# Optimization experiments

Measured on AMD Instinct MI355X. Metric: run time of the kernel, lower is better.

Reference implementation:

```python
import jax, jax.numpy as jnp
import numpy as np

N_EMBD = 1024
N_HEAD = 16
HEAD_SIZE = 64
BLOCK_SIZE = 2048


def setup_inputs() -> dict:
    key = jax.random.key(0)
    ks = jax.random.split(key, 5)
    B, T = 2, 2048
    s_attn = 1.0 / np.sqrt(N_EMBD)
    x = jax.random.normal(ks[0], (B, T, N_EMBD), dtype=jnp.float32)
    W_attn = jax.random.normal(ks[1], (N_EMBD, 3 * N_EMBD), dtype=jnp.float32) * s_attn
    b_attn = jnp.zeros((3 * N_EMBD,), dtype=jnp.float32)
    W_proj = jax.random.normal(ks[2], (N_EMBD, N_EMBD), dtype=jnp.float32) * s_attn
    b_proj = jnp.zeros((N_EMBD,), dtype=jnp.float32)
    return {"x": x, "W_attn": W_attn, "b_attn": b_attn, "W_proj": W_proj, "b_proj": b_proj}


def reference(x, W_attn, b_attn, W_proj, b_proj):
    B, T, C = x.shape
    H, D = N_HEAD, HEAD_SIZE
    qkv = x @ W_attn + b_attn                      # [B, T, 3C]
    q, k, v = jnp.split(qkv, 3, axis=-1)
    # [B, H, T, D]
    q = q.reshape(B, T, H, D).transpose(0, 2, 1, 3)
    k = k.reshape(B, T, H, D).transpose(0, 2, 1, 3)
    v = v.reshape(B, T, H, D).transpose(0, 2, 1, 3)
    scores = jnp.einsum("bhqd,bhkd->bhqk", q, k) / jnp.sqrt(jnp.float32(D))
    causal = jnp.tril(jnp.ones((T, T), dtype=bool))
    scores = jnp.where(causal[None, None, :, :], scores, -jnp.inf)
    weights = jax.nn.softmax(scores, axis=-1)
    attn = jnp.einsum("bhqk,bhkd->bhqd", weights, v)  # [B, H, T, D]
    attn = attn.transpose(0, 2, 1, 3).reshape(B, T, C)
    return attn @ W_proj + b_proj
```

## Files before the change

### kernel.cpp

```cpp
#include <hip/hip_runtime.h>
#include <hip/hip_bf16.h>

#define NE 1024
#define NH 16
#define HD 64
#define TSEQ 2048
#define BATCH 2

typedef __attribute__((ext_vector_type(8))) short bf16x8;
typedef __attribute__((ext_vector_type(4))) float f32x4;
typedef __attribute__((ext_vector_type(4))) unsigned int u32x4;
typedef unsigned short u16;
typedef unsigned int u32;

__device__ inline u16 f2bf(float f) {
    __hip_bfloat16 h = __float2bfloat16(f);
    return *reinterpret_cast<u16*>(&h);
}

__device__ inline u32 cvt_pk_bf16(float lo, float hi) {
    u32 r;
    asm("v_cvt_pk_bf16_f32 %0, %1, %2" : "=v"(r) : "v"(lo), "v"(hi));
    return r;
}

#define GLD16(gptr, lptr)                                                        \
    __builtin_amdgcn_global_load_lds(                                            \
        (const __attribute__((address_space(1))) void*)(gptr),                   \
        (__attribute__((address_space(3))) void*)(lptr), 16, 0, 0)

__global__ void k_f32_to_bf16(const float* __restrict__ in, u16* __restrict__ out, int n4) {
    int i = blockIdx.x * blockDim.x + threadIdx.x;
    int stride = gridDim.x * blockDim.x;
    for (; i < n4; i += stride) {
        float4 v = reinterpret_cast<const float4*>(in)[i];
        ushort4 o;
        o.x = f2bf(v.x); o.y = f2bf(v.y); o.z = f2bf(v.z); o.w = f2bf(v.w);
        reinterpret_cast<ushort4*>(out)[i] = o;
    }
}

__global__ void k_transpose_bf16(const float* __restrict__ in, u16* __restrict__ out,
                                 int K, int N) {
    __shared__ float tile[32][33];
    int bn = blockIdx.x * 32;
    int bk = blockIdx.y * 32;
    int tx = threadIdx.x, ty = threadIdx.y;
#pragma unroll
    for (int i = 0; i < 32; i += 8)
        tile[ty + i][tx] = in[(size_t)(bk + ty + i) * N + bn + tx];
    __syncthreads();
#pragma unroll
    for (int i = 0; i < 32; i += 8)
        out[(size_t)(bn + ty + i) * K + bk + tx] = f2bf(tile[tx][ty + i]);
}

template <int MODE>
__global__ __launch_bounds__(256, 2) void k_gemm_bt(
    const u16* __restrict__ A, const u16* __restrict__ Bt,
    const float* __restrict__ bias, void* __restrict__ outp,
    int M, int N, int K) {
    __shared__ __align__(16) u16 As[128 * 32];
    __shared__ __align__(16) u16 Bs[128 * 32];
    const int l = threadIdx.x & 63;
    const int w = threadIdx.x >> 6;
    const int m0 = blockIdx.x * 128;
    const int n0 = blockIdx.y * 128;
    const int wr = w >> 1, wc = w & 1;

    f32x4 acc[4][4] = {};
    const int nkt = K >> 5;
    for (int kt = 0; kt < nkt; ++kt) {
        __syncthreads();
#pragma unroll
        for (int i = 0; i < 2; ++i) {
            int c = w * 2 + i;
            const u16* gA = A + (size_t)(m0 + c * 16 + (l >> 2)) * K + (kt << 5) + (l & 3) * 8;
            const u16* gB = Bt + (size_t)(n0 + c * 16 + (l >> 2)) * K + (kt << 5) + (l & 3) * 8;
            GLD16(gA, As + c * 512);
            GLD16(gB, Bs + c * 512);
        }
        __syncthreads();
        bf16x8 af[4], bfr[4];
#pragma unroll
        for (int mi = 0; mi < 4; ++mi)
            af[mi] = *reinterpret_cast<const bf16x8*>(As + (wr * 64 + mi * 16 + (l & 15)) * 32 + (l >> 4) * 8);
#pragma unroll
        for (int ni = 0; ni < 4; ++ni)
            bfr[ni] = *reinterpret_cast<const bf16x8*>(Bs + (wc * 64 + ni * 16 + (l & 15)) * 32 + (l >> 4) * 8);
#pragma unroll
        for (int mi = 0; mi < 4; ++mi)
#pragma unroll
            for (int ni = 0; ni < 4; ++ni)
                acc[mi][ni] = __builtin_amdgcn_mfma_f32_16x16x32_bf16(af[mi], bfr[ni], acc[mi][ni], 0, 0, 0);
    }

    if (MODE == 1) {
        float* C = (float*)outp;
#pragma unroll
        for (int mi = 0; mi < 4; ++mi)
#pragma unroll
            for (int ni = 0; ni < 4; ++ni) {
                int n = n0 + wc * 64 + ni * 16 + (l & 15);
                float bv = bias[n];
#pragma unroll
                for (int r = 0; r < 4; ++r) {
                    int m = m0 + wr * 64 + mi * 16 + (l >> 4) * 4 + r;
                    C[(size_t)m * N + n] = acc[mi][ni][r] + bv;
                }
            }
    } else {
        u16* qkv = (u16*)outp;
        const size_t headsz = (size_t)BATCH * NH * TSEQ * HD;
#pragma unroll
        for (int mi = 0; mi < 4; ++mi)
#pragma unroll
            for (int ni = 0; ni < 4; ++ni) {
                int n = n0 + wc * 64 + ni * 16 + (l & 15);
                float bv = bias[n];
                int which = n >> 10;
                int c = n & 1023;
                int h = c >> 6, d = c & 63;
#pragma unroll
                for (int r = 0; r < 4; ++r) {
                    int m = m0 + wr * 64 + mi * 16 + (l >> 4) * 4 + r;
                    int b = m >> 11, t = m & 2047;
                    float v = acc[mi][ni][r] + bv;
                    size_t dst;
                    if (which == 2)
                        dst = 2 * headsz + ((size_t)(b * NH + h) * HD + d) * TSEQ + t;
                    else
                        dst = (size_t)which * headsz + ((size_t)(b * NH + h) * TSEQ + t) * HD + d;
                    qkv[dst] = f2bf(v);
                }
            }
    }
}

__global__ __launch_bounds__(256, 4) void k_attn(
    const u16* __restrict__ qb, const u16* __restrict__ kb, const u16* __restrict__ vtb,
    u16* __restrict__ attn_out) {
    __shared__ __align__(16) u16 Ks[2][64 * 64];
    __shared__ __align__(16) u16 Vs[2][64 * 64];
    const int l = threadIdx.x & 63;
    const int w = threadIdx.x >> 6;
    const int g = l >> 4, l15 = l & 15;

    const int bid = blockIdx.x;
    const int i = bid >> 5;
    const int bh = bid & 31;
    const int hi = i >> 3, lo = i & 7;
    const int j = hi * 8 + ((hi & 1) ? (7 - lo) : lo);
    const int q0 = j * 64;

    const int b = bh >> 4, h = bh & 15;
    const size_t base = (size_t)bh * TSEQ * HD;
    const u16* Q = qb + base;
    const u16* Kg = kb + base;
    const u16* Vg = vtb + base;

    const int lrow8 = l >> 3;
    const int lchunk = (l & 7) ^ lrow8;

    const int qrow = q0 + w * 16 + l15;
    bf16x8 qa[2];
    qa[0] = *reinterpret_cast<const bf16x8*>(Q + (size_t)qrow * HD + g * 8);
    qa[1] = *reinterpret_cast<const bf16x8*>(Q + (size_t)qrow * HD + 32 + g * 8);

    float mrow = -1e30f, lsum = 0.f;
    f32x4 o[4] = {};

    const int ntiles = j + 1;
    const float SC = 0.125f * 1.44269504f;
    const float THRU = 8.0f / SC;

    const int srcA = ((2 * g) & 3) * 16 + l15;
    const int srcB = ((2 * g + 1) & 3) * 16 + l15;
    const bool losel = (g < 2);

#pragma unroll
    for (int i2 = 0; i2 < 2; ++i2) {
        int c = w * 2 + i2;
        GLD16(Kg + (size_t)(c * 8 + lrow8) * HD + lchunk * 8, &Ks[0][c * 512]);
        GLD16(Vg + (size_t)(c * 8 + lrow8) * TSEQ + lchunk * 8, &Vs[0][c * 512]);
    }
    __syncthreads();

    int cur = 0;
    for (int kt = 0; kt < ntiles; ++kt) {
        if (kt + 1 < ntiles) {
            int nb = cur ^ 1;
#pragma unroll
            for (int i2 = 0; i2 < 2; ++i2) {
                int c = w * 2 + i2;
                GLD16(Kg + (size_t)((kt + 1) * 64 + c * 8 + lrow8) * HD + lchunk * 8,
                      &Ks[nb][c * 512]);
                GLD16(Vg + (size_t)(c * 8 + lrow8) * TSEQ + (kt + 1) * 64 + lchunk * 8,
                      &Vs[nb][c * 512]);
            }
        }
        const u16* Kc = Ks[cur];
        const u16* Vc = Vs[cur];

        f32x4 s[4] = {};
        __builtin_amdgcn_s_setprio(1);
#pragma unroll
        for (int f = 0; f < 4; ++f)
#pragma unroll
            for (int ks = 0; ks < 2; ++ks) {
                bf16x8 bk = *reinterpret_cast<const bf16x8*>(
                    Kc + (f * 16 + l15) * 64 + (((ks * 4 + g) ^ (l15 & 7)) * 8));
                s[f] = __builtin_amdgcn_mfma_f32_16x16x32_bf16(bk, qa[ks], s[f], 0, 0, 0);
            }
        __builtin_amdgcn_s_setprio(0);

        if (kt == ntiles - 1) {
#pragma unroll
            for (int f = 0; f < 4; ++f)
#pragma unroll
                for (int r = 0; r < 4; ++r) {
                    int kg = (kt << 6) + f * 16 + g * 4 + r;
                    if (kg > qrow) s[f][r] = -1e30f;
                }
        }

        float rmax = -1e30f;
#pragma unroll
        for (int f = 0; f < 4; ++f)
            rmax = fmaxf(rmax, fmaxf(fmaxf(s[f][0], s[f][1]), fmaxf(s[f][2], s[f][3])));
        rmax = fmaxf(rmax, __shfl_xor(rmax, 16));
        rmax = fmaxf(rmax, __shfl_xor(rmax, 32));

        if (__any(rmax - mrow > THRU)) {
            float mnew = fmaxf(mrow, rmax);
            float alpha = exp2f((mrow - mnew) * SC);
            mrow = mnew;
            lsum *= alpha;
#pragma unroll
            for (int nf = 0; nf < 4; ++nf)
#pragma unroll
                for (int r = 0; r < 4; ++r)
                    o[nf][r] *= alpha;
        }
        const float mc = mrow * SC;

        float pe[4][4];
        float rsum = 0.f;
#pragma unroll
        for (int f = 0; f < 4; ++f)
#pragma unroll
            for (int r = 0; r < 4; ++r) {
                float v = exp2f(__builtin_fmaf(s[f][r], SC, -mc));
                pe[f][r] = v;
                rsum += v;
            }
        rsum += __shfl_xor(rsum, 16);
        rsum += __shfl_xor(rsum, 32);
        lsum += rsum;

        u32 w0[4], w1[4];
#pragma unroll
        for (int f = 0; f < 4; ++f) {
            w0[f] = cvt_pk_bf16(pe[f][0], pe[f][1]);
            w1[f] = cvt_pk_bf16(pe[f][2], pe[f][3]);
        }

        __builtin_amdgcn_s_setprio(1);
#pragma unroll
        for (int ks = 0; ks < 2; ++ks) {
            u32 t00 = (u32)__shfl((int)w0[2 * ks], srcA);
            u32 t01 = (u32)__shfl((int)w0[2 * ks + 1], srcA);
            u32 t10 = (u32)__shfl((int)w1[2 * ks], srcA);
            u32 t11 = (u32)__shfl((int)w1[2 * ks + 1], srcA);
            u32 t20 = (u32)__shfl((int)w0[2 * ks], srcB);
            u32 t21 = (u32)__shfl((int)w0[2 * ks + 1], srcB);
            u32 t30 = (u32)__shfl((int)w1[2 * ks], srcB);
            u32 t31 = (u32)__shfl((int)w1[2 * ks + 1], srcB);
            u32x4 bb;
            bb.x = losel ? t00 : t01;
            bb.y = losel ? t10 : t11;
            bb.z = losel ? t20 : t21;
            bb.w = losel ? t30 : t31;
            bf16x8 pb = __builtin_bit_cast(bf16x8, bb);
#pragma unroll
            for (int nf = 0; nf < 4; ++nf) {
                bf16x8 bv = *reinterpret_cast<const bf16x8*>(
                    Vc + (nf * 16 + l15) * 64 + (((ks * 4 + g) ^ (l15 & 7)) * 8));
                o[nf] = __builtin_amdgcn_mfma_f32_16x16x32_bf16(bv, pb, o[nf], 0, 0, 0);
            }
        }
        __builtin_amdgcn_s_setprio(0);
        __syncthreads();
        cur ^= 1;
    }

    const float inv = 1.0f / lsum;
    u16* orow = attn_out + (size_t)(b * TSEQ + qrow) * NE + h * HD;
#pragma unroll
    for (int nf = 0; nf < 4; ++nf) {
        int d0 = nf * 16 + g * 4;
        u32 p01 = cvt_pk_bf16(o[nf][0] * inv, o[nf][1] * inv);
        u32 p23 = cvt_pk_bf16(o[nf][2] * inv, o[nf][3] * inv);
        *reinterpret_cast<u32*>(orow + d0) = p01;
        *reinterpret_cast<u32*>(orow + d0 + 2) = p23;
    }
}

extern "C" void kernel_launch(void* const* d_in, const int* in_sizes, int n_in,
                              void* d_out, int out_size, void* d_ws, size_t ws_size,
                              hipStream_t stream) {
    const float* x = (const float*)d_in[0];
    const float* W_attn = (const float*)d_in[1];
    const float* b_attn = (const float*)d_in[2];
    const float* W_proj = (const float*)d_in[3];
    const float* b_proj = (const float*)d_in[4];
    float* out = (float*)d_out;

    char* ws = (char*)d_ws;
    u16* xb   = (u16*)(ws);
    u16* WaT  = (u16*)(ws + 8u * 1024 * 1024);
    u16* WpT  = (u16*)(ws + 14u * 1024 * 1024);
    u16* qkvb = (u16*)(ws + 16u * 1024 * 1024);
    u16* attn = (u16*)(ws + 40u * 1024 * 1024);

    const int M = BATCH * TSEQ;

    k_f32_to_bf16<<<2048, 256, 0, stream>>>(x, xb, (M * NE) / 4);
    k_transpose_bf16<<<dim3(3 * NE / 32, NE / 32), dim3(32, 8), 0, stream>>>(W_attn, WaT, NE, 3 * NE);
    k_transpose_bf16<<<dim3(NE / 32, NE / 32), dim3(32, 8), 0, stream>>>(W_proj, WpT, NE, NE);

    k_gemm_bt<0><<<dim3(M / 128, (3 * NE) / 128), 256, 0, stream>>>(xb, WaT, b_attn, qkvb, M, 3 * NE, NE);

    const size_t headsz = (size_t)BATCH * NH * TSEQ * HD;
    k_attn<<<dim3(32 * BATCH * NH), 256, 0, stream>>>(qkvb, qkvb + headsz, qkvb + 2 * headsz, attn);

    k_gemm_bt<1><<<dim3(M / 128, NE / 128), 256, 0, stream>>>(attn, WpT, b_proj, out, M, NE, NE);
}
```

Before: 134.4 us.

## Split attention KV tiles across warps with per-warp staging and LDS merge

The attention kernel now has each of the four warps process all 64 query rows of a block against a strided subset of KV tiles (split-K within the block), instead of each warp owning 16 query rows and sharing double-buffered K/V tiles. Each warp loads its own K/V tile into private LDS and waits synchronously. Partial max, sum and output are merged through LDS at the end with rescaling. Blocks are ordered longest-first. This removes per-tile block barriers and reuses each K/V fragment across four query groups, but it drops load/compute overlap, raises register pressure (launch bounds lowered to 2) and adds a bf16 round-trip on the partial outputs.

```diff
diff --git a/kernel.cpp b/kernel.cpp
--- a/kernel.cpp
+++ b/kernel.cpp
@@ -16,6 +16,11 @@
 __device__ inline u16 f2bf(float f) {
     __hip_bfloat16 h = __float2bfloat16(f);
     return *reinterpret_cast<u16*>(&h);
+}
+
+__device__ inline float bf2f(u32 bits) {
+    u32 v = bits << 16;
+    return __builtin_bit_cast(float, v);
 }
 
 __device__ inline u32 cvt_pk_bf16(float lo, float hi) {
@@ -137,22 +142,18 @@
     }
 }
 
-__global__ __launch_bounds__(256, 4) void k_attn(
+__global__ __launch_bounds__(256, 2) void k_attn(
     const u16* __restrict__ qb, const u16* __restrict__ kb, const u16* __restrict__ vtb,
     u16* __restrict__ attn_out) {
-    __shared__ __align__(16) u16 Ks[2][64 * 64];
-    __shared__ __align__(16) u16 Vs[2][64 * 64];
+    __shared__ __align__(16) u16 stage[4][8192];
     const int l = threadIdx.x & 63;
     const int w = threadIdx.x >> 6;
     const int g = l >> 4, l15 = l & 15;
 
     const int bid = blockIdx.x;
-    const int i = bid >> 5;
+    const int t = 31 - (bid >> 5);
     const int bh = bid & 31;
-    const int hi = i >> 3, lo = i & 7;
-    const int j = hi * 8 + ((hi & 1) ? (7 - lo) : lo);
-    const int q0 = j * 64;
-
+    const int q0 = t * 64;
     const int b = bh >> 4, h = bh & 15;
     const size_t base = (size_t)bh * TSEQ * HD;
     const u16* Q = qb + base;
@@ -162,55 +163,54 @@
     const int lrow8 = l >> 3;
     const int lchunk = (l & 7) ^ lrow8;
 
-    const int qrow = q0 + w * 16 + l15;
-    bf16x8 qa[2];
-    qa[0] = *reinterpret_cast<const bf16x8*>(Q + (size_t)qrow * HD + g * 8);
-    qa[1] = *reinterpret_cast<const bf16x8*>(Q + (size_t)qrow * HD + 32 + g * 8);
-
-    float mrow = -1e30f, lsum = 0.f;
-    f32x4 o[4] = {};
-
-    const int ntiles = j + 1;
+    u16* myK = &stage[w][0];
+    u16* myV = &stage[w][4096];
+
+    bf16x8 qa[4][2];
+#pragma unroll
+    for (int qn = 0; qn < 4; ++qn)
+#pragma unroll
+        for (int ks = 0; ks < 2; ++ks)
+            qa[qn][ks] = *reinterpret_cast<const bf16x8*>(
+                Q + (size_t)(q0 + qn * 16 + l15) * HD + ks * 32 + g * 8);
+    asm volatile("s_waitcnt vmcnt(0)" ::: "memory");
+
+    float m[4], lsum[4];
+    f32x4 o[4][4] = {};
+#pragma unroll
+    for (int r = 0; r < 4; ++r) { m[r] = -1e30f; lsum[r] = 0.f; }
+
+    const int ntiles = t + 1;
     const float SC = 0.125f * 1.44269504f;
-    const float THRU = 8.0f / SC;
+    const float THRU = 44.3614f;
 
     const int srcA = ((2 * g) & 3) * 16 + l15;
     const int srcB = ((2 * g + 1) & 3) * 16 + l15;
     const bool losel = (g < 2);
 
-#pragma unroll
-    for (int i2 = 0; i2 < 2; ++i2) {
-        int c = w * 2 + i2;
-        GLD16(Kg + (size_t)(c * 8 + lrow8) * HD + lchunk * 8, &Ks[0][c * 512]);
-        GLD16(Vg + (size_t)(c * 8 + lrow8) * TSEQ + lchunk * 8, &Vs[0][c * 512]);
-    }
-    __syncthreads();
-
-    int cur = 0;
-    for (int kt = 0; kt < ntiles; ++kt) {
-        if (kt + 1 < ntiles) {
-            int nb = cur ^ 1;
-#pragma unroll
-            for (int i2 = 0; i2 < 2; ++i2) {
-                int c = w * 2 + i2;
-                GLD16(Kg + (size_t)((kt + 1) * 64 + c * 8 + lrow8) * HD + lchunk * 8,
-                      &Ks[nb][c * 512]);
-                GLD16(Vg + (size_t)(c * 8 + lrow8) * TSEQ + (kt + 1) * 64 + lchunk * 8,
-                      &Vs[nb][c * 512]);
-            }
-        }
-        const u16* Kc = Ks[cur];
-        const u16* Vc = Vs[cur];
-
-        f32x4 s[4] = {};
+    for (int kt = w; kt < ntiles; kt += 4) {
+        __builtin_amdgcn_sched_barrier(0);
+        const u16* Kt = Kg + (size_t)kt * 64 * HD;
+#pragma unroll
+        for (int c = 0; c < 8; ++c)
+            GLD16(Kt + (size_t)(c * 8 + lrow8) * HD + lchunk * 8, myK + c * 512);
+#pragma unroll
+        for (int c = 0; c < 8; ++c)
+            GLD16(Vg + (size_t)(c * 8 + lrow8) * TSEQ + kt * 64 + lchunk * 8, myV + c * 512);
+        asm volatile("s_waitcnt vmcnt(0)" ::: "memory");
+        __builtin_amdgcn_sched_barrier(0);
+
+        f32x4 s[4][4] = {};
         __builtin_amdgcn_s_setprio(1);
 #pragma unroll
-        for (int f = 0; f < 4; ++f)
-#pragma unroll
-            for (int ks = 0; ks < 2; ++ks) {
+        for (int ks = 0; ks < 2; ++ks)
+#pragma unroll
+            for (int f = 0; f < 4; ++f) {
                 bf16x8 bk = *reinterpret_cast<const bf16x8*>(
-                    Kc + (f * 16 + l15) * 64 + (((ks * 4 + g) ^ (l15 & 7)) * 8));
-                s[f] = __builtin_amdgcn_mfma_f32_16x16x32_bf16(bk, qa[ks], s[f], 0, 0, 0);
+                    myK + (f * 16 + l15) * 64 + (((ks * 4 + g) ^ (l15 & 7)) * 8));
+#pragma unroll
+                for (int qn = 0; qn < 4; ++qn)
+                    s[f][qn] = __builtin_amdgcn_mfma_f32_16x16x32_bf16(bk, qa[qn][ks], s[f][qn], 0, 0, 0);
             }
         __builtin_amdgcn_s_setprio(0);
 
@@ -218,91 +218,139 @@
 #pragma unroll
             for (int f = 0; f < 4; ++f)
 #pragma unroll
+                for (int qn = 0; qn < 4; ++qn)
+#pragma unroll
+                    for (int r = 0; r < 4; ++r) {
+                        int kg = (kt << 6) + f * 16 + g * 4 + r;
+                        int qg = q0 + qn * 16 + l15;
+                        if (kg > qg) s[f][qn][r] = -1e30f;
+                    }
+        }
+
+        u32 pk0[4][4], pk1[4][4];
+#pragma unroll
+        for (int qn = 0; qn < 4; ++qn) {
+            float rmax = -1e30f;
+#pragma unroll
+            for (int f = 0; f < 4; ++f)
+                rmax = fmaxf(rmax, fmaxf(fmaxf(s[f][qn][0], s[f][qn][1]),
+                                         fmaxf(s[f][qn][2], s[f][qn][3])));
+            rmax = fmaxf(rmax, __shfl_xor(rmax, 16));
+            rmax = fmaxf(rmax, __shfl_xor(rmax, 32));
+
+            if (__any(rmax - m[qn] > THRU)) {
+                float mnew = fmaxf(m[qn], rmax);
+                float alpha = exp2f((m[qn] - mnew) * SC);
+                m[qn] = mnew;
+                lsum[qn] *= alpha;
+#pragma unroll
+                for (int nf = 0; nf < 4; ++nf)
+#pragma unroll
+                    for (int r = 0; r < 4; ++r)
+                        o[qn][nf][r] *= alpha;
+            }
+            const float mc = m[qn] * SC;
+            float rsum = 0.f;
+            float pe[4][4];
+#pragma unroll
+            for (int f = 0; f < 4; ++f)
+#pragma unroll
                 for (int r = 0; r < 4; ++r) {
-                    int kg = (kt << 6) + f * 16 + g * 4 + r;
-                    if (kg > qrow) s[f][r] = -1e30f;
+                    float v = exp2f(__builtin_fmaf(s[f][qn][r], SC, -mc));
+                    pe[f][r] = v;
+                    rsum += v;
                 }
-        }
-
-        float rmax = -1e30f;
-#pragma unroll
-        for (int f = 0; f < 4; ++f)
-            rmax = fmaxf(rmax, fmaxf(fmaxf(s[f][0], s[f][1]), fmaxf(s[f][2], s[f][3])));
-        rmax = fmaxf(rmax, __shfl_xor(rmax, 16));
-        rmax = fmaxf(rmax, __shfl_xor(rmax, 32));
-
-        if (__any(rmax - mrow > THRU)) {
-            float mnew = fmaxf(mrow, rmax);
-            float alpha = exp2f((mrow - mnew) * SC);
-            mrow = mnew;
-            lsum *= alpha;
-#pragma unroll
-            for (int nf = 0; nf < 4; ++nf)
-#pragma unroll
-                for (int r = 0; r < 4; ++r)
-                    o[nf][r] *= alpha;
-        }
-        const float mc = mrow * SC;
-
-        float pe[4][4];
-        float rsum = 0.f;
-#pragma unroll
-        for (int f = 0; f < 4; ++f)
-#pragma unroll
-            for (int r = 0; r < 4; ++r) {
-                float v = exp2f(__builtin_fmaf(s[f][r], SC, -mc));
-                pe[f][r] = v;
-                rsum += v;
-            }
-        rsum += __shfl_xor(rsum, 16);
-        rsum += __shfl_xor(rsum, 32);
-        lsum += rsum;
-
-        u32 w0[4], w1[4];
-#pragma unroll
-        for (int f = 0; f < 4; ++f) {
-            w0[f] = cvt_pk_bf16(pe[f][0], pe[f][1]);
-            w1[f] = cvt_pk_bf16(pe[f][2], pe[f][3]);
+            rsum += __shfl_xor(rsum, 16);
+            rsum += __shfl_xor(rsum, 32);
+            lsum[qn] += rsum;
+#pragma unroll
+            for (int f = 0; f < 4; ++f) {
+                pk0[qn][f] = cvt_pk_bf16(pe[f][0], pe[f][1]);
+                pk1[qn][f] = cvt_pk_bf16(pe[f][2], pe[f][3]);
+            }
         }
 
         __builtin_amdgcn_s_setprio(1);
 #pragma unroll
         for (int ks = 0; ks < 2; ++ks) {
-            u32 t00 = (u32)__shfl((int)w0[2 * ks], srcA);
-            u32 t01 = (u32)__shfl((int)w0[2 * ks + 1], srcA);
-            u32 t10 = (u32)__shfl((int)w1[2 * ks], srcA);
-            u32 t11 = (u32)__shfl((int)w1[2 * ks + 1], srcA);
-            u32 t20 = (u32)__shfl((int)w0[2 * ks], srcB);
-            u32 t21 = (u32)__shfl((int)w0[2 * ks + 1], srcB);
-            u32 t30 = (u32)__shfl((int)w1[2 * ks], srcB);
-            u32 t31 = (u32)__shfl((int)w1[2 * ks + 1], srcB);
-            u32x4 bb;
-            bb.x = losel ? t00 : t01;
-            bb.y = losel ? t10 : t11;
-            bb.z = losel ? t20 : t21;
-            bb.w = losel ? t30 : t31;
-            bf16x8 pb = __builtin_bit_cast(bf16x8, bb);
+            bf16x8 pb[4];
+#pragma unroll
+            for (int qn = 0; qn < 4; ++qn) {
+                u32 t00 = (u32)__shfl((int)pk0[qn][2 * ks], srcA);
+                u32 t01 = (u32)__shfl((int)pk0[qn][2 * ks + 1], srcA);
+                u32 t10 = (u32)__shfl((int)pk1[qn][2 * ks], srcA);
+                u32 t11 = (u32)__shfl((int)pk1[qn][2 * ks + 1], srcA);
+                u32 t20 = (u32)__shfl((int)pk0[qn][2 * ks], srcB);
+                u32 t21 = (u32)__shfl((int)pk0[qn][2 * ks + 1], srcB);
+                u32 t30 = (u32)__shfl((int)pk1[qn][2 * ks], srcB);
+                u32 t31 = (u32)__shfl((int)pk1[qn][2 * ks + 1], srcB);
+                u32x4 bb;
+                bb.x = losel ? t00 : t01;
+                bb.y = losel ? t10 : t11;
+                bb.z = losel ? t20 : t21;
+                bb.w = losel ? t30 : t31;
+                pb[qn] = __builtin_bit_cast(bf16x8, bb);
+            }
 #pragma unroll
             for (int nf = 0; nf < 4; ++nf) {
                 bf16x8 bv = *reinterpret_cast<const bf16x8*>(
-                    Vc + (nf * 16 + l15) * 64 + (((ks * 4 + g) ^ (l15 & 7)) * 8));
-                o[nf] = __builtin_amdgcn_mfma_f32_16x16x32_bf16(bv, pb, o[nf], 0, 0, 0);
+                    myV + (nf * 16 + l15) * 64 + (((ks * 4 + g) ^ (l15 & 7)) * 8));
+#pragma unroll
+                for (int qn = 0; qn < 4; ++qn)
+                    o[qn][nf] = __builtin_amdgcn_mfma_f32_16x16x32_bf16(bv, pb[qn], o[qn][nf], 0, 0, 0);
             }
         }
         __builtin_amdgcn_s_setprio(0);
-        __syncthreads();
-        cur ^= 1;
-    }
-
-    const float inv = 1.0f / lsum;
-    u16* orow = attn_out + (size_t)(b * TSEQ + qrow) * NE + h * HD;
-#pragma unroll
-    for (int nf = 0; nf < 4; ++nf) {
-        int d0 = nf * 16 + g * 4;
-        u32 p01 = cvt_pk_bf16(o[nf][0] * inv, o[nf][1] * inv);
-        u32 p23 = cvt_pk_bf16(o[nf][2] * inv, o[nf][3] * inv);
-        *reinterpret_cast<u32*>(orow + d0) = p01;
-        *reinterpret_cast<u32*>(orow + d0 + 2) = p23;
+    }
+
+    __syncthreads();
+    u16* om = &stage[0][0];
+    float* ml = (float*)(&stage[0][0] + 16896);
+
+#pragma unroll
+    for (int qn = 0; qn < 4; ++qn) {
+        int q = qn * 16 + l15;
+        if (g == 0) {
+            ml[(w * 2 + 0) * 64 + q] = m[qn];
+            ml[(w * 2 + 1) * 64 + q] = lsum[qn];
+        }
+#pragma unroll
+        for (int nf = 0; nf < 4; ++nf) {
+            u32* dst = (u32*)&om[(w * 64 + q) * 66 + nf * 16 + g * 4];
+            dst[0] = cvt_pk_bf16(o[qn][nf][0], o[qn][nf][1]);
+            dst[1] = cvt_pk_bf16(o[qn][nf][2], o[qn][nf][3]);
+        }
+    }
+    __syncthreads();
+
+#pragma unroll
+    for (int qn = 0; qn < 4; ++qn) {
+        int q = qn * 16 + l15;
+        float mw[4], lw[4];
+#pragma unroll
+        for (int ws = 0; ws < 4; ++ws) {
+            mw[ws] = ml[(ws * 2 + 0) * 64 + q];
+            lw[ws] = ml[(ws * 2 + 1) * 64 + q];
+        }
+        float M = fmaxf(fmaxf(mw[0], mw[1]), fmaxf(mw[2], mw[3]));
+        float L = 0.f, a0 = 0.f, a1 = 0.f, a2 = 0.f, a3 = 0.f;
+#pragma unroll
+        for (int ws = 0; ws < 4; ++ws) {
+            float sc = exp2f((mw[ws] - M) * SC);
+            L += lw[ws] * sc;
+            const u32* src = (const u32*)&om[(ws * 64 + q) * 66 + w * 16 + g * 4];
+            u32 x = src[0], y = src[1];
+            a0 += bf2f(x & 0xffffu) * sc;
+            a1 += bf2f(x >> 16) * sc;
+            a2 += bf2f(y & 0xffffu) * sc;
+            a3 += bf2f(y >> 16) * sc;
+        }
+        float inv = 1.f / L;
+        u32 p01 = cvt_pk_bf16(a0 * inv, a1 * inv);
+        u32 p23 = cvt_pk_bf16(a2 * inv, a3 * inv);
+        u16* orow = attn_out + (size_t)(b * TSEQ + q0 + q) * NE + h * HD + w * 16 + g * 4;
+        *reinterpret_cast<u32*>(orow) = p01;
+        *reinterpret_cast<u32*>(orow + 2) = p23;
     }
 }
 
@@ -332,7 +380,7 @@
     k_gemm_bt<0><<<dim3(M / 128, (3 * NE) / 128), 256, 0, stream>>>(xb, WaT, b_attn, qkvb, M, 3 * NE, NE);
 
     const size_t headsz = (size_t)BATCH * NH * TSEQ * HD;
-    k_attn<<<dim3(32 * BATCH * NH), 256, 0, stream>>>(qkvb, qkvb + headsz, qkvb + 2 * headsz, attn);
+    k_attn<<<dim3(32 * 32), 256, 0, stream>>>(qkvb, qkvb + headsz, qkvb + 2 * headsz, attn);
 
     k_gemm_bt<1><<<dim3(M / 128, NE / 128), 256, 0, stream>>>(attn, WpT, b_proj, out, M, NE, NE);
 }
```

Result: no change. 134.8 us (+0.3%).

## Split attention KV range into two halves and merge partial softmax results

Applied to the files above, without the earlier changes.

Each query tile's causal KV range is split across two blocks, which doubles the grid and launches the longest tiles first. A separate merge kernel then combines the partial outputs using the saved row max and sum. The aim is better load balance and occupancy across CUs for the causal attention. In exchange it writes the partial O in bf16, adds an extra kernel launch and extra memory traffic, and loses some precision in the unnormalised partials. The rescale threshold constant also changes; it is an absolute score value in place of the old 8/SC, which evaluates to the same number.

```diff
diff --git a/kernel.cpp b/kernel.cpp
--- a/kernel.cpp
+++ b/kernel.cpp
@@ -6,6 +6,7 @@
 #define HD 64
 #define TSEQ 2048
 #define BATCH 2
+#define MB (1024u * 1024u)
 
 typedef __attribute__((ext_vector_type(8))) short bf16x8;
 typedef __attribute__((ext_vector_type(4))) float f32x4;
@@ -16,6 +17,11 @@
 __device__ inline u16 f2bf(float f) {
     __hip_bfloat16 h = __float2bfloat16(f);
     return *reinterpret_cast<u16*>(&h);
+}
+
+__device__ inline float bf2f(u32 bits) {
+    u32 v = bits << 16;
+    return __builtin_bit_cast(float, v);
 }
 
 __device__ inline u32 cvt_pk_bf16(float lo, float hi) {
@@ -139,7 +145,7 @@
 
 __global__ __launch_bounds__(256, 4) void k_attn(
     const u16* __restrict__ qb, const u16* __restrict__ kb, const u16* __restrict__ vtb,
-    u16* __restrict__ attn_out) {
+    u16* __restrict__ oPart, float* __restrict__ mlPart) {
     __shared__ __align__(16) u16 Ks[2][64 * 64];
     __shared__ __align__(16) u16 Vs[2][64 * 64];
     const int l = threadIdx.x & 63;
@@ -147,13 +153,14 @@
     const int g = l >> 4, l15 = l & 15;
 
     const int bid = blockIdx.x;
-    const int i = bid >> 5;
+    const int t = 31 - (bid >> 6);
+    const int half = (bid >> 5) & 1;
     const int bh = bid & 31;
-    const int hi = i >> 3, lo = i & 7;
-    const int j = hi * 8 + ((hi & 1) ? (7 - lo) : lo);
-    const int q0 = j * 64;
-
-    const int b = bh >> 4, h = bh & 15;
+    const int q0 = t * 64;
+    const int nA = (t + 2) >> 1;
+    const int ktLo = half ? nA : 0;
+    const int ktHi = half ? (t + 1) : nA;
+
     const size_t base = (size_t)bh * TSEQ * HD;
     const u16* Q = qb + base;
     const u16* Kg = kb + base;
@@ -170,140 +177,179 @@
     float mrow = -1e30f, lsum = 0.f;
     f32x4 o[4] = {};
 
-    const int ntiles = j + 1;
     const float SC = 0.125f * 1.44269504f;
-    const float THRU = 8.0f / SC;
+    const float THRU = 44.3614f;
 
     const int srcA = ((2 * g) & 3) * 16 + l15;
     const int srcB = ((2 * g + 1) & 3) * 16 + l15;
     const bool losel = (g < 2);
 
-#pragma unroll
-    for (int i2 = 0; i2 < 2; ++i2) {
-        int c = w * 2 + i2;
-        GLD16(Kg + (size_t)(c * 8 + lrow8) * HD + lchunk * 8, &Ks[0][c * 512]);
-        GLD16(Vg + (size_t)(c * 8 + lrow8) * TSEQ + lchunk * 8, &Vs[0][c * 512]);
-    }
-    __syncthreads();
-
-    int cur = 0;
-    for (int kt = 0; kt < ntiles; ++kt) {
-        if (kt + 1 < ntiles) {
-            int nb = cur ^ 1;
-#pragma unroll
-            for (int i2 = 0; i2 < 2; ++i2) {
-                int c = w * 2 + i2;
-                GLD16(Kg + (size_t)((kt + 1) * 64 + c * 8 + lrow8) * HD + lchunk * 8,
-                      &Ks[nb][c * 512]);
-                GLD16(Vg + (size_t)(c * 8 + lrow8) * TSEQ + (kt + 1) * 64 + lchunk * 8,
-                      &Vs[nb][c * 512]);
-            }
+    if (ktLo < ktHi) {
+#pragma unroll
+        for (int i2 = 0; i2 < 2; ++i2) {
+            int c = w * 2 + i2;
+            GLD16(Kg + (size_t)(ktLo * 64 + c * 8 + lrow8) * HD + lchunk * 8, &Ks[0][c * 512]);
+            GLD16(Vg + (size_t)(c * 8 + lrow8) * TSEQ + ktLo * 64 + lchunk * 8, &Vs[0][c * 512]);
         }
-        const u16* Kc = Ks[cur];
-        const u16* Vc = Vs[cur];
-
-        f32x4 s[4] = {};
-        __builtin_amdgcn_s_setprio(1);
-#pragma unroll
-        for (int f = 0; f < 4; ++f)
+        __syncthreads();
+
+        int cur = 0;
+        for (int kt = ktLo; kt < ktHi; ++kt) {
+            if (kt + 1 < ktHi) {
+                int nb = cur ^ 1;
+#pragma unroll
+                for (int i2 = 0; i2 < 2; ++i2) {
+                    int c = w * 2 + i2;
+                    GLD16(Kg + (size_t)((kt + 1) * 64 + c * 8 + lrow8) * HD + lchunk * 8,
+                          &Ks[nb][c * 512]);
+                    GLD16(Vg + (size_t)(c * 8 + lrow8) * TSEQ + (kt + 1) * 64 + lchunk * 8,
+                          &Vs[nb][c * 512]);
+                }
+            }
+            const u16* Kc = Ks[cur];
+            const u16* Vc = Vs[cur];
+
+            f32x4 s[4] = {};
+            __builtin_amdgcn_s_setprio(1);
+#pragma unroll
+            for (int f = 0; f < 4; ++f)
+#pragma unroll
+                for (int ks = 0; ks < 2; ++ks) {
+                    bf16x8 bk = *reinterpret_cast<const bf16x8*>(
+                        Kc + (f * 16 + l15) * 64 + (((ks * 4 + g) ^ (l15 & 7)) * 8));
+                    s[f] = __builtin_amdgcn_mfma_f32_16x16x32_bf16(bk, qa[ks], s[f], 0, 0, 0);
+                }
+            __builtin_amdgcn_s_setprio(0);
+
+            if (kt == t) {
+#pragma unroll
+                for (int f = 0; f < 4; ++f)
+#pragma unroll
+                    for (int r = 0; r < 4; ++r) {
+                        int kg = (kt << 6) + f * 16 + g * 4 + r;
+                        if (kg > qrow) s[f][r] = -1e30f;
+                    }
+            }
+
+            float rmax = -1e30f;
+#pragma unroll
+            for (int f = 0; f < 4; ++f)
+                rmax = fmaxf(rmax, fmaxf(fmaxf(s[f][0], s[f][1]), fmaxf(s[f][2], s[f][3])));
+            rmax = fmaxf(rmax, __shfl_xor(rmax, 16));
+            rmax = fmaxf(rmax, __shfl_xor(rmax, 32));
+
+            if (__any(rmax - mrow > THRU)) {
+                float mnew = fmaxf(mrow, rmax);
+                float alpha = exp2f((mrow - mnew) * SC);
+                mrow = mnew;
+                lsum *= alpha;
+#pragma unroll
+                for (int nf = 0; nf < 4; ++nf)
+#pragma unroll
+                    for (int r = 0; r < 4; ++r)
+                        o[nf][r] *= alpha;
+            }
+            const float mc = mrow * SC;
+
+            float pe[4][4];
+            float rsum = 0.f;
+#pragma unroll
+            for (int f = 0; f < 4; ++f)
+#pragma unroll
+                for (int r = 0; r < 4; ++r) {
+                    float v = exp2f(__builtin_fmaf(s[f][r], SC, -mc));
+                    pe[f][r] = v;
+                    rsum += v;
+                }
+            rsum += __shfl_xor(rsum, 16);
+            rsum += __shfl_xor(rsum, 32);
+            lsum += rsum;
+
+            u32 w0[4], w1[4];
+#pragma unroll
+            for (int f = 0; f < 4; ++f) {
+                w0[f] = cvt_pk_bf16(pe[f][0], pe[f][1]);
+                w1[f] = cvt_pk_bf16(pe[f][2], pe[f][3]);
+            }
+
+            __builtin_amdgcn_s_setprio(1);
 #pragma unroll
             for (int ks = 0; ks < 2; ++ks) {
-                bf16x8 bk = *reinterpret_cast<const bf16x8*>(
-                    Kc + (f * 16 + l15) * 64 + (((ks * 4 + g) ^ (l15 & 7)) * 8));
-                s[f] = __builtin_amdgcn_mfma_f32_16x16x32_bf16(bk, qa[ks], s[f], 0, 0, 0);
-            }
-        __builtin_amdgcn_s_setprio(0);
-
-        if (kt == ntiles - 1) {
-#pragma unroll
-            for (int f = 0; f < 4; ++f)
-#pragma unroll
-                for (int r = 0; r < 4; ++r) {
-                    int kg = (kt << 6) + f * 16 + g * 4 + r;
-                    if (kg > qrow) s[f][r] = -1e30f;
-                }
+                u32 t00 = (u32)__shfl((int)w0[2 * ks], srcA);
+                u32 t01 = (u32)__shfl((int)w0[2 * ks + 1], srcA);
+                u32 t10 = (u32)__shfl((int)w1[2 * ks], srcA);
+                u32 t11 = (u32)__shfl((int)w1[2 * ks + 1], srcA);
+                u32 t20 = (u32)__shfl((int)w0[2 * ks], srcB);
+                u32 t21 = (u32)__shfl((int)w0[2 * ks + 1], srcB);
+                u32 t30 = (u32)__shfl((int)w1[2 * ks], srcB);
+                u32 t31 = (u32)__shfl((int)w1[2 * ks + 1], srcB);
+                u32x4 bb;
+                bb.x = losel ? t00 : t01;
+                bb.y = losel ? t10 : t11;
+                bb.z = losel ? t20 : t21;
+                bb.w = losel ? t30 : t31;
+                bf16x8 pb = __builtin_bit_cast(bf16x8, bb);
+#pragma unroll
+                for (int nf = 0; nf < 4; ++nf) {
+                    bf16x8 bv = *reinterpret_cast<const bf16x8*>(
+                        Vc + (nf * 16 + l15) * 64 + (((ks * 4 + g) ^ (l15 & 7)) * 8));
+                    o[nf] = __builtin_amdgcn_mfma_f32_16x16x32_bf16(bv, pb, o[nf], 0, 0, 0);
+                }
+            }
+            __builtin_amdgcn_s_setprio(0);
+            __syncthreads();
+            cur ^= 1;
         }
-
-        float rmax = -1e30f;
-#pragma unroll
-        for (int f = 0; f < 4; ++f)
-            rmax = fmaxf(rmax, fmaxf(fmaxf(s[f][0], s[f][1]), fmaxf(s[f][2], s[f][3])));
-        rmax = fmaxf(rmax, __shfl_xor(rmax, 16));
-        rmax = fmaxf(rmax, __shfl_xor(rmax, 32));
-
-        if (__any(rmax - mrow > THRU)) {
-            float mnew = fmaxf(mrow, rmax);
-            float alpha = exp2f((mrow - mnew) * SC);
-            mrow = mnew;
-            lsum *= alpha;
-#pragma unroll
-            for (int nf = 0; nf < 4; ++nf)
-#pragma unroll
-                for (int r = 0; r < 4; ++r)
-                    o[nf][r] *= alpha;
-        }
-        const float mc = mrow * SC;
-
-        float pe[4][4];
-        float rsum = 0.f;
-#pragma unroll
-        for (int f = 0; f < 4; ++f)
-#pragma unroll
-            for (int r = 0; r < 4; ++r) {
-                float v = exp2f(__builtin_fmaf(s[f][r], SC, -mc));
-                pe[f][r] = v;
-                rsum += v;
-            }
-        rsum += __shfl_xor(rsum, 16);
-        rsum += __shfl_xor(rsum, 32);
-        lsum += rsum;
-
-        u32 w0[4], w1[4];
-#pragma unroll
-        for (int f = 0; f < 4; ++f) {
-            w0[f] = cvt_pk_bf16(pe[f][0], pe[f][1]);
-            w1[f] = cvt_pk_bf16(pe[f][2], pe[f][3]);
-        }
-
-        __builtin_amdgcn_s_setprio(1);
-#pragma unroll
-        for (int ks = 0; ks < 2; ++ks) {
-            u32 t00 = (u32)__shfl((int)w0[2 * ks], srcA);
-            u32 t01 = (u32)__shfl((int)w0[2 * ks + 1], srcA);
-            u32 t10 = (u32)__shfl((int)w1[2 * ks], srcA);
-            u32 t11 = (u32)__shfl((int)w1[2 * ks + 1], srcA);
-            u32 t20 = (u32)__shfl((int)w0[2 * ks], srcB);
-            u32 t21 = (u32)__shfl((int)w0[2 * ks + 1], srcB);
-            u32 t30 = (u32)__shfl((int)w1[2 * ks], srcB);
-            u32 t31 = (u32)__shfl((int)w1[2 * ks + 1], srcB);
-            u32x4 bb;
-            bb.x = losel ? t00 : t01;
-            bb.y = losel ? t10 : t11;
-            bb.z = losel ? t20 : t21;
-            bb.w = losel ? t30 : t31;
-            bf16x8 pb = __builtin_bit_cast(bf16x8, bb);
-#pragma unroll
-            for (int nf = 0; nf < 4; ++nf) {
-                bf16x8 bv = *reinterpret_cast<const bf16x8*>(
-                    Vc + (nf * 16 + l15) * 64 + (((ks * 4 + g) ^ (l15 & 7)) * 8));
-                o[nf] = __builtin_amdgcn_mfma_f32_16x16x32_bf16(bv, pb, o[nf], 0, 0, 0);
-            }
-        }
-        __builtin_amdgcn_s_setprio(0);
-        __syncthreads();
-        cur ^= 1;
-    }
-
-    const float inv = 1.0f / lsum;
-    u16* orow = attn_out + (size_t)(b * TSEQ + qrow) * NE + h * HD;
+    }
+
+    const size_t oHalf = (size_t)32 * TSEQ * HD;
+    u16* oRow = oPart + half * oHalf + ((size_t)bh * TSEQ + qrow) * HD;
 #pragma unroll
     for (int nf = 0; nf < 4; ++nf) {
         int d0 = nf * 16 + g * 4;
-        u32 p01 = cvt_pk_bf16(o[nf][0] * inv, o[nf][1] * inv);
-        u32 p23 = cvt_pk_bf16(o[nf][2] * inv, o[nf][3] * inv);
-        *reinterpret_cast<u32*>(orow + d0) = p01;
-        *reinterpret_cast<u32*>(orow + d0 + 2) = p23;
-    }
+        u32 p01 = cvt_pk_bf16(o[nf][0], o[nf][1]);
+        u32 p23 = cvt_pk_bf16(o[nf][2], o[nf][3]);
+        *reinterpret_cast<u32*>(oRow + d0) = p01;
+        *reinterpret_cast<u32*>(oRow + d0 + 2) = p23;
+    }
+    if (g == 0) {
+        float* mlH = mlPart + half * ((size_t)32 * 2 * TSEQ);
+        mlH[((size_t)bh * 2 + 0) * TSEQ + qrow] = mrow;
+        mlH[((size_t)bh * 2 + 1) * TSEQ + qrow] = lsum;
+    }
+}
+
+__global__ void k_merge(const u16* __restrict__ oPart, const float* __restrict__ mlPart,
+                        u16* __restrict__ attn_out) {
+    const float SC = 0.125f * 1.44269504f;
+    int tid = blockIdx.x * blockDim.x + threadIdx.x;
+    int dblk = tid & 7;
+    int q = (tid >> 3) & 2047;
+    int bh = tid >> 14;
+    const size_t oHalf = (size_t)32 * TSEQ * HD;
+    const size_t mlHalf = (size_t)32 * 2 * TSEQ;
+    float mA = mlPart[((size_t)bh * 2 + 0) * TSEQ + q];
+    float lA = mlPart[((size_t)bh * 2 + 1) * TSEQ + q];
+    float mB = mlPart[mlHalf + ((size_t)bh * 2 + 0) * TSEQ + q];
+    float lB = mlPart[mlHalf + ((size_t)bh * 2 + 1) * TSEQ + q];
+    float M = fmaxf(mA, mB);
+    float eA = exp2f((mA - M) * SC);
+    float eB = exp2f((mB - M) * SC);
+    float invL = 1.0f / (lA * eA + lB * eB);
+    float fA = eA * invL, fB = eB * invL;
+    const u32* pa = (const u32*)(oPart + ((size_t)bh * TSEQ + q) * HD + dblk * 8);
+    const u32* pb = (const u32*)(oPart + oHalf + ((size_t)bh * TSEQ + q) * HD + dblk * 8);
+    u32 outw[4];
+#pragma unroll
+    for (int i = 0; i < 4; ++i) {
+        u32 a = pa[i], b = pb[i];
+        float lo = bf2f(a & 0xffffu) * fA + bf2f(b & 0xffffu) * fB;
+        float hi = bf2f(a >> 16) * fA + bf2f(b >> 16) * fB;
+        outw[i] = cvt_pk_bf16(lo, hi);
+    }
+    int bb = bh >> 4, h = bh & 15;
+    u16* dst = attn_out + ((size_t)(bb * TSEQ + q) * NE) + h * HD + dblk * 8;
+    *reinterpret_cast<u32x4*>(dst) = *reinterpret_cast<const u32x4*>(outw);
 }
 
 extern "C" void kernel_launch(void* const* d_in, const int* in_sizes, int n_in,
@@ -317,11 +363,13 @@
     float* out = (float*)d_out;
 
     char* ws = (char*)d_ws;
-    u16* xb   = (u16*)(ws);
-    u16* WaT  = (u16*)(ws + 8u * 1024 * 1024);
-    u16* WpT  = (u16*)(ws + 14u * 1024 * 1024);
-    u16* qkvb = (u16*)(ws + 16u * 1024 * 1024);
-    u16* attn = (u16*)(ws + 40u * 1024 * 1024);
+    u16* xb     = (u16*)(ws);
+    u16* WaT    = (u16*)(ws + 8 * MB);
+    u16* qkvb   = (u16*)(ws + 16 * MB);
+    u16* attn   = (u16*)(ws + 40 * MB);
+    u16* WpT    = (u16*)(ws + 48 * MB);
+    float* mlP  = (float*)(ws + 50 * MB);
+    u16* oPart  = (u16*)(ws);
 
     const int M = BATCH * TSEQ;
 
@@ -332,7 +380,9 @@
     k_gemm_bt<0><<<dim3(M / 128, (3 * NE) / 128), 256, 0, stream>>>(xb, WaT, b_attn, qkvb, M, 3 * NE, NE);
 
     const size_t headsz = (size_t)BATCH * NH * TSEQ * HD;
-    k_attn<<<dim3(32 * BATCH * NH), 256, 0, stream>>>(qkvb, qkvb + headsz, qkvb + 2 * headsz, attn);
+    k_attn<<<dim3(32 * 2 * 32), 256, 0, stream>>>(qkvb, qkvb + headsz, qkvb + 2 * headsz, oPart, mlP);
+
+    k_merge<<<dim3((32 * TSEQ * 8) / 256), 256, 0, stream>>>(oPart, mlP, attn);
 
     k_gemm_bt<1><<<dim3(M / 128, NE / 128), 256, 0, stream>>>(attn, WpT, b_proj, out, M, NE, NE);
 }
```

Result: faster. 130.2 us (-3.1%).
